# Kernel optimization log

Hardware: AMD Instinct MI355X
Metric: run time of the kernel (lower is better)

The kernel has to match this reference:

```python
import jax, jax.numpy as jnp
import numpy as np

N_NODES = 100000
EPS = 1e-12


def _sage_layer(x, W, b, src, dst):
    # Linear projection: [N, d_in] @ [d_in, d_out]^T
    h = x @ W.T + b
    # F.normalize: row-wise L2 normalize with eps clamp
    norm = jnp.linalg.norm(h, axis=1, keepdims=True)
    h = h / jnp.maximum(norm, EPS)
    # scatter-mean aggregation: message x_j = h[src], reduce at dst
    msg = h[src]                                            # [E, d_out] gather
    agg = jax.ops.segment_sum(msg, dst, num_segments=N_NODES)
    cnt = jax.ops.segment_sum(jnp.ones((dst.shape[0], 1), h.dtype), dst,
                              num_segments=N_NODES)
    return agg / jnp.maximum(cnt, 1.0)
    # NOTE: the torch code does `x += bias` AFTER computing `out` and returns
    # `out`, so the bias parameter of GraphSage never affects the output.


def setup_inputs() -> dict:
    key = jax.random.key(0)
    ks = jax.random.split(key, 12)
    d_in, d_h, d_out = 128, 128, 40
    E = 3200000
    s = lambda k, shape, fan: jax.random.normal(k, shape, jnp.float32) * (1.0 / np.sqrt(fan))
    return {
        "x": jax.random.normal(ks[0], (N_NODES, d_in), jnp.float32),
        "edge_index": jax.random.randint(ks[1], (2, E), 0, N_NODES, jnp.int64),
        "W0": s(ks[2], (d_h, d_in), d_in), "b0": jnp.zeros((d_h,), jnp.float32),
        "W1": s(ks[3], (d_h, d_h), d_h),  "b1": jnp.zeros((d_h,), jnp.float32),
        "W2": s(ks[4], (d_h, d_h), d_h),  "b2": jnp.zeros((d_h,), jnp.float32),
        "Wp1": s(ks[5], (d_h, d_h), d_h), "bp1": jnp.zeros((d_h,), jnp.float32),
        "Wp2": s(ks[6], (d_out, d_h), d_h), "bp2": jnp.zeros((d_out,), jnp.float32),
    }


def reference(x, edge_index, W0, b0, W1, b1, W2, b2, Wp1, bp1, Wp2, bp2):
    src, dst = edge_index[0], edge_index[1]
    h = x
    for W, b in ((W0, b0), (W1, b1), (W2, b2)):
        h = _sage_layer(h, W, b, src, dst)
        h = jax.nn.relu(h)
        # dropout p=0.0 -> identity
    h = h @ Wp1.T + bp1
    h = h @ Wp2.T + bp2
    return jax.nn.log_softmax(h, axis=1)
```

## Files before the change

### kernel.cpp

```cpp
#include <hip/hip_runtime.h>
#include <cmath>

#define NN 100000
#define NB 512
#define NLOC 196
#define CAP 7168
#define CHUNK 8192

typedef unsigned int uint32;
typedef unsigned short ushort16;
typedef __attribute__((ext_vector_type(8))) short short8;
typedef __attribute__((ext_vector_type(4))) float f32x4;
typedef __attribute__((ext_vector_type(2))) float f32x2;

#if defined(__has_builtin)
#if __has_builtin(__builtin_amdgcn_cvt_pk_f32_fp8) && __has_builtin(__builtin_amdgcn_cvt_pk_fp8_f32)
#define HAS_HW_FP8 1
#endif
#endif

__device__ __forceinline__ ushort16 f2bf(float f) {
    uint32 b = __float_as_uint(f);
    uint32 r = (b + 0x7FFFu + ((b >> 16) & 1u)) >> 16;
    return (ushort16)r;
}

#ifdef HAS_HW_FP8
__device__ __forceinline__ uint32 pack4_e4m3(float a, float b, float c, float d) {
    int v = 0;
    v = __builtin_amdgcn_cvt_pk_fp8_f32(a, b, v, false);
    v = __builtin_amdgcn_cvt_pk_fp8_f32(c, d, v, true);
    return (uint32)v;
}
#else
__device__ __forceinline__ uint32 enc1_e4m3(float f) {
    uint32 bits = __float_as_uint(f);
    uint32 s = (bits >> 24) & 0x80u;
    float a = fabsf(f);
    if (a >= 448.f) return s | 0x7Eu;
    if (a < 0.0009765625f) return s;
    if (a < 0.015625f) return s | (uint32)rintf(a * 512.f);
    int e; float m = frexpf(a, &e);
    uint32 q = (uint32)rintf(m * 16.f);
    if (q == 16) { q = 8; e++; }
    return s | ((uint32)(e + 6) << 3) | (q - 8);
}
__device__ __forceinline__ uint32 pack4_e4m3(float a, float b, float c, float d) {
    return enc1_e4m3(a) | (enc1_e4m3(b) << 8) | (enc1_e4m3(c) << 16) | (enc1_e4m3(d) << 24);
}
#endif

#ifdef HAS_HW_FP8
#define DEC_PK(u, w) __builtin_amdgcn_cvt_pk_f32_fp8((int)(u), (w))
#else
__device__ __forceinline__ float dec1_e4m3(uint32 u) {
    uint32 s = (u & 0x80u) << 24;
    uint32 em = u & 0x7Fu;
    if (em >= 8)
        return __uint_as_float(s | (((em >> 3) + 120u) << 23) | ((em & 7u) << 20));
    return ((u & 0x80u) ? -1.f : 1.f) * (float)em * 0.001953125f;
}
__device__ __forceinline__ f32x2 DEC_PK(uint32 u, bool w) {
    uint32 h = w ? (u >> 16) : u;
    f32x2 r; r.x = dec1_e4m3(h & 0xFF); r.y = dec1_e4m3((h >> 8) & 0xFF);
    return r;
}
#endif

__global__ void conv_weights(const float* __restrict__ W0, const float* __restrict__ W1,
                             const float* __restrict__ W2, const float* __restrict__ Wp1,
                             const float* __restrict__ Wp2,
                             uint2* __restrict__ o0, uint2* __restrict__ o1,
                             uint2* __restrict__ o2, uint2* __restrict__ o3,
                             ushort16* __restrict__ o4, int* __restrict__ cursor) {
    int i = blockIdx.x * 256 + threadIdx.x;
    if (i < 16384) {
        const int m = i >> 12;
        const int q = i & 4095;
        const float* src = (m == 0) ? W0 : (m == 1) ? W1 : (m == 2) ? W2 : Wp1;
        uint2* dst = (m == 0) ? o0 : (m == 1) ? o1 : (m == 2) ? o2 : o3;
        const float4 v = *((const float4*)src + q);
        ushort16 o[4] = {f2bf(v.x), f2bf(v.y), f2bf(v.z), f2bf(v.w)};
        dst[q] = *(uint2*)o;
    } else if (i < 16384 + 1536) {
        const int q = i - 16384;
        const int e = q * 4;
        const int j = e >> 7, k = e & 127;
        ushort16 o[4];
#pragma unroll
        for (int c = 0; c < 4; c++) o[c] = (j < 40) ? f2bf(Wp2[j * 128 + k + c]) : (ushort16)0;
        *(uint2*)(o4 + e) = *(uint2*)o;
    } else if (i < 16384 + 1536 + NB) {
        cursor[i - 16384 - 1536] = 0;
    }
}

__global__ __launch_bounds__(512) void csr_k1(const int* __restrict__ srcv,
                                              const int* __restrict__ dstv, int E,
                                              int* __restrict__ cursor,
                                              uint32* __restrict__ ebuf) {
    __shared__ int lhist[NB];
    __shared__ int lstart[NB];
    __shared__ int lbase[NB];
    __shared__ int lcnt[NB];
    __shared__ uint32 sval[CHUNK];
    __shared__ int sgoff[CHUNK];
    const int t = threadIdx.x;
    const int e0 = blockIdx.x * CHUNK;
    const int e1 = min(e0 + CHUNK, E);
    const int n = e1 - e0;

    if (t < NB) { lhist[t] = 0; lcnt[t] = 0; }
    __syncthreads();
    for (int i = e0 + t; i < e1; i += 512)
        atomicAdd(&lhist[dstv[i] / NLOC], 1);
    __syncthreads();

    const int v = lhist[t];
    lstart[t] = v;
    __syncthreads();
    for (int off = 1; off < NB; off <<= 1) {
        int x = (t >= off) ? lstart[t - off] : 0;
        __syncthreads();
        lstart[t] += x;
        __syncthreads();
    }
    const int excl = lstart[t] - v;
    lstart[t] = excl;
    lbase[t] = v ? atomicAdd(&cursor[t], v) : 0;
    __syncthreads();

    for (int i = e0 + t; i < e1; i += 512) {
        const int d = dstv[i];
        const int s = srcv[i];
        const int b = d / NLOC;
        const int pos = atomicAdd(&lcnt[b], 1);
        const int wpos = lbase[b] + pos;
        const int idx = lstart[b] + pos;
        sval[idx] = (uint32)s | ((uint32)(d - b * NLOC) << 17);
        sgoff[idx] = (wpos < CAP) ? (b * CAP + wpos) : -1;
    }
    __syncthreads();

    for (int k = t; k < n; k += 512) {
        const int g = sgoff[k];
        if (g >= 0) ebuf[g] = sval[k];
    }
}

__global__ __launch_bounds__(NB) void scanb_k(const int* __restrict__ cursor,
                                              int* __restrict__ bstart) {
    __shared__ int sd[NB];
    const int t = threadIdx.x;
    const int v = cursor[t];
    sd[t] = v;
    __syncthreads();
    for (int off = 1; off < NB; off <<= 1) {
        int x = (t >= off) ? sd[t - off] : 0;
        __syncthreads();
        sd[t] += x;
        __syncthreads();
    }
    bstart[t] = sd[t] - v;
}

__global__ __launch_bounds__(512) void csr_k2(const uint32* __restrict__ ebuf,
                                              const int* __restrict__ cursor,
                                              const int* __restrict__ bstart,
                                              int* __restrict__ rowptr,
                                              int* __restrict__ colv, int Etot) {
    __shared__ int sd[256];
    __shared__ int loc[256];
    __shared__ int cnt[256];
    __shared__ uint32 eld[CAP];
    __shared__ uint32 sorted[CAP];
    const int b = blockIdx.x;
    const int t = threadIdx.x;
    const int n = min(cursor[b], CAP);
    const int n0 = b * NLOC;
    const int nloc = max(0, min(NN - n0, NLOC));
    const int bst = bstart[b];
    const uint32* seg = ebuf + (size_t)b * CAP;

    if (t < 256) { sd[t] = 0; cnt[t] = 0; }
    __syncthreads();
    for (int i = t; i < n; i += 512) {
        const uint32 p = seg[i];
        eld[i] = p;
        atomicAdd(&sd[p >> 17], 1);
    }
    __syncthreads();
    int v = 0;
    if (t < 256) v = sd[t];
    __syncthreads();
    for (int off = 1; off < 256; off <<= 1) {
        int x = 0;
        if (t < 256 && t >= off) x = sd[t - off];
        __syncthreads();
        if (t < 256) sd[t] += x;
        __syncthreads();
    }
    if (t < 256) loc[t] = sd[t] - v;
    __syncthreads();
    if (t < nloc) rowptr[n0 + t] = bst + loc[t];
    if (b == 0 && t == 0) rowptr[NN] = Etot;

    for (int i = t; i < n; i += 512) {
        const uint32 p = eld[i];
        const int l = p >> 17;
        const int pos = atomicAdd(&cnt[l], 1);
        sorted[loc[l] + pos] = p & 0x1FFFF;
    }
    __syncthreads();
    for (int i = t; i < n; i += 512)
        colv[bst + i] = (int)(sorted[i] << 7);
}

template <int F32IN>
__global__ __launch_bounds__(256) void lin_mfma(const void* __restrict__ Xin,
                                                const ushort16* __restrict__ Wb,
                                                const float* __restrict__ bias,
                                                unsigned char* __restrict__ Y8) {
    __shared__ short8 wls[2048];
    const int t = threadIdx.x;
    const int l = t & 63;
    const int l15 = l & 15, lh = l >> 4;
    const int rbase = blockIdx.x * 64 + (t >> 6) * 16;
    int arow = rbase + l15;
    if (arow >= NN) arow = NN - 1;

#pragma unroll
    for (int it = 0; it < 8; it++) {
        const int idx = it * 256 + t;
        const int j = idx >> 8, kk = (idx >> 6) & 3, ll = idx & 63;
        wls[idx] = *(const short8*)((const ushort16*)Wb + (size_t)(j * 16 + (ll & 15)) * 128 + kk * 32 + (ll >> 4) * 8);
    }

    short8 a[4];
    if (F32IN) {
        const float* ap = (const float*)Xin + (size_t)arow * 128 + lh * 8;
#pragma unroll
        for (int kk = 0; kk < 4; kk++) {
            const float4 p0 = *(const float4*)(ap + kk * 32);
            const float4 p1 = *(const float4*)(ap + kk * 32 + 4);
            ushort16 o[8] = {f2bf(p0.x), f2bf(p0.y), f2bf(p0.z), f2bf(p0.w),
                             f2bf(p1.x), f2bf(p1.y), f2bf(p1.z), f2bf(p1.w)};
            a[kk] = *(short8*)o;
        }
    } else {
        const ushort16* ap = (const ushort16*)Xin + (size_t)arow * 128 + lh * 8;
#pragma unroll
        for (int kk = 0; kk < 4; kk++) a[kk] = *(const short8*)(ap + kk * 32);
    }

    __syncthreads();

    f32x4 acc[8];
#pragma unroll
    for (int j = 0; j < 8; j++) acc[j] = (f32x4){0.f, 0.f, 0.f, 0.f};

#pragma unroll
    for (int kk = 0; kk < 4; kk++)
#pragma unroll
        for (int j = 0; j < 8; j++)
            acc[j] = __builtin_amdgcn_mfma_f32_16x16x32_bf16(wls[j * 256 + kk * 64 + l], a[kk], acc[j], 0, 0, 0);

    float v[8][4];
    float ssq = 0.f;
#pragma unroll
    for (int j = 0; j < 8; j++) {
        const float4 bv = *(const float4*)(bias + j * 16 + lh * 4);
        v[j][0] = acc[j][0] + bv.x;
        v[j][1] = acc[j][1] + bv.y;
        v[j][2] = acc[j][2] + bv.z;
        v[j][3] = acc[j][3] + bv.w;
        ssq += v[j][0] * v[j][0] + v[j][1] * v[j][1] + v[j][2] * v[j][2] + v[j][3] * v[j][3];
    }
    ssq += __shfl_xor(ssq, 16, 64);
    ssq += __shfl_xor(ssq, 32, 64);
    const float sc = 1.f / fmaxf(sqrtf(ssq), 1e-12f);

    const int row = rbase + l15;
    if (row < NN) {
        unsigned char* yp = Y8 + (size_t)row * 128;
#pragma unroll
        for (int j = 0; j < 8; j++) {
            const uint32 p = pack4_e4m3(v[j][0] * sc, v[j][1] * sc, v[j][2] * sc, v[j][3] * sc);
            *(uint32*)(yp + j * 16 + lh * 4) = p;
        }
    }
}

__global__ __launch_bounds__(256) void agg_k(const unsigned char* __restrict__ hp,
                                             const int* __restrict__ rowptr,
                                             const int* __restrict__ colv,
                                             ushort16* __restrict__ outp) {
    const int lane = threadIdx.x & 63;
    const int q = lane >> 4;
    const int l16 = lane & 15;
    const int wid = blockIdx.x * 4 + (threadIdx.x >> 6);
    const int nw = gridDim.x * 4;

    for (int node = wid; node < NN; node += nw) {
        const int s = rowptr[node], e = rowptr[node + 1];
        f32x2 a2[4];
#pragma unroll
        for (int j = 0; j < 4; j++) a2[j] = (f32x2){0.f, 0.f};
        const unsigned char* bp = hp + l16 * 8;

        int i = s + q;
        for (; i + 12 < e; i += 16) {
            const int c0 = colv[i];
            const int c1 = colv[i + 4];
            const int c2 = colv[i + 8];
            const int c3 = colv[i + 12];
            const uint2 u0 = *(const uint2*)(bp + (size_t)(uint32)c0);
            const uint2 u1 = *(const uint2*)(bp + (size_t)(uint32)c1);
            const uint2 u2 = *(const uint2*)(bp + (size_t)(uint32)c2);
            const uint2 u3 = *(const uint2*)(bp + (size_t)(uint32)c3);
#pragma unroll
            for (int r = 0; r < 4; r++) {
                const uint2 u = (r == 0) ? u0 : (r == 1) ? u1 : (r == 2) ? u2 : u3;
                a2[0] += DEC_PK(u.x, false);
                a2[1] += DEC_PK(u.x, true);
                a2[2] += DEC_PK(u.y, false);
                a2[3] += DEC_PK(u.y, true);
            }
        }
        for (; i < e; i += 4) {
            const uint2 u = *(const uint2*)(bp + (size_t)(uint32)colv[i]);
            a2[0] += DEC_PK(u.x, false);
            a2[1] += DEC_PK(u.x, true);
            a2[2] += DEC_PK(u.y, false);
            a2[3] += DEC_PK(u.y, true);
        }

        float av[8] = {a2[0].x, a2[0].y, a2[1].x, a2[1].y,
                       a2[2].x, a2[2].y, a2[3].x, a2[3].y};
#pragma unroll
        for (int j = 0; j < 8; j++) {
            av[j] += __shfl_xor(av[j], 16, 64);
            av[j] += __shfl_xor(av[j], 32, 64);
        }

        if (q == 0) {
            const float inv = 1.f / fmaxf((float)(e - s), 1.f);
            ushort16 o[8];
#pragma unroll
            for (int j = 0; j < 8; j++) o[j] = f2bf(fmaxf(av[j] * inv, 0.f));
            *(uint4*)(outp + (size_t)node * 128 + l16 * 8) = *(uint4*)o;
        }
    }
}

__global__ __launch_bounds__(256) void post_mfma(const ushort16* __restrict__ Bb,
                                                 const ushort16* __restrict__ W1b,
                                                 const float* __restrict__ bp1,
                                                 const ushort16* __restrict__ W2b,
                                                 const float* __restrict__ bp2,
                                                 float* __restrict__ Out) {
    __shared__ ushort16 hls[64 * 128];
    const int t = threadIdx.x;
    const int w = t >> 6;
    const int l = t & 63;
    const int l15 = l & 15, lh = l >> 4;
    const int rl = w * 16 + l15;
    const int rbase = blockIdx.x * 64 + w * 16;
    int arow = rbase + l15;
    if (arow >= NN) arow = NN - 1;

    {
        f32x4 acc[8];
#pragma unroll
        for (int j = 0; j < 8; j++) acc[j] = (f32x4){0.f, 0.f, 0.f, 0.f};
        const ushort16* ap = Bb + (size_t)arow * 128 + lh * 8;
#pragma unroll
        for (int kk = 0; kk < 4; kk++) {
            const short8 a = *(const short8*)(ap + kk * 32);
#pragma unroll
            for (int j = 0; j < 8; j++) {
                const short8 b = *(const short8*)(W1b + (size_t)(j * 16 + l15) * 128 + kk * 32 + lh * 8);
                acc[j] = __builtin_amdgcn_mfma_f32_16x16x32_bf16(b, a, acc[j], 0, 0, 0);
            }
        }
        char* lp = (char*)hls;
#pragma unroll
        for (int j = 0; j < 8; j++) {
            const float4 bv = *(const float4*)(bp1 + j * 16 + lh * 4);
            ushort16 o[4] = {f2bf(acc[j][0] + bv.x), f2bf(acc[j][1] + bv.y),
                             f2bf(acc[j][2] + bv.z), f2bf(acc[j][3] + bv.w)};
            const int byte = (rl * 256 + j * 32 + lh * 8) ^ ((rl & 7) << 4);
            *(uint2*)(lp + byte) = *(uint2*)o;
        }
    }
    __syncthreads();

    {
        f32x4 acc[3];
#pragma unroll
        for (int j = 0; j < 3; j++) acc[j] = (f32x4){0.f, 0.f, 0.f, 0.f};
        const char* lp = (const char*)hls;
#pragma unroll
        for (int kk = 0; kk < 4; kk++) {
            const int byte = (rl * 256 + kk * 64 + lh * 16) ^ ((rl & 7) << 4);
            const short8 a = *(const short8*)(lp + byte);
#pragma unroll
            for (int j = 0; j < 3; j++) {
                const short8 b = *(const short8*)(W2b + (size_t)(j * 16 + l15) * 128 + kk * 32 + lh * 8);
                acc[j] = __builtin_amdgcn_mfma_f32_16x16x32_bf16(b, a, acc[j], 0, 0, 0);
            }
        }

        float v[3][4];
        float m = -1e30f;
#pragma unroll
        for (int j = 0; j < 3; j++) {
            const bool val = (j < 2) || (lh < 2);
            if (val) {
                const float4 bv = *(const float4*)(bp2 + j * 16 + lh * 4);
                v[j][0] = acc[j][0] + bv.x;
                v[j][1] = acc[j][1] + bv.y;
                v[j][2] = acc[j][2] + bv.z;
                v[j][3] = acc[j][3] + bv.w;
#pragma unroll
                for (int r = 0; r < 4; r++) m = fmaxf(m, v[j][r]);
            } else {
#pragma unroll
                for (int r = 0; r < 4; r++) v[j][r] = -1e30f;
            }
        }
        m = fmaxf(m, __shfl_xor(m, 16, 64));
        m = fmaxf(m, __shfl_xor(m, 32, 64));
        float se = 0.f;
#pragma unroll
        for (int j = 0; j < 3; j++)
#pragma unroll
            for (int r = 0; r < 4; r++) se += expf(v[j][r] - m);
        se += __shfl_xor(se, 16, 64);
        se += __shfl_xor(se, 32, 64);
        const float lse = logf(se) + m;

        const int row = rbase + l15;
        if (row < NN) {
            float* op = Out + (size_t)row * 40;
#pragma unroll
            for (int j = 0; j < 3; j++) {
                if (j == 2 && lh >= 2) continue;
                float4 o;
                o.x = v[j][0] - lse; o.y = v[j][1] - lse;
                o.z = v[j][2] - lse; o.w = v[j][3] - lse;
                *(float4*)(op + j * 16 + lh * 4) = o;
            }
        }
    }
}

extern "C" void kernel_launch(void* const* d_in, const int* in_sizes, int n_in,
                              void* d_out, int out_size, void* d_ws, size_t ws_size,
                              hipStream_t stream) {
    const float* x   = (const float*)d_in[0];
    const int*   ei  = (const int*)d_in[1];
    const float* W0  = (const float*)d_in[2];
    const float* b0  = (const float*)d_in[3];
    const float* W1  = (const float*)d_in[4];
    const float* b1  = (const float*)d_in[5];
    const float* W2  = (const float*)d_in[6];
    const float* b2  = (const float*)d_in[7];
    const float* Wp1 = (const float*)d_in[8];
    const float* bp1 = (const float*)d_in[9];
    const float* Wp2 = (const float*)d_in[10];
    const float* bp2 = (const float*)d_in[11];
    float* out = (float*)d_out;

    const int E = in_sizes[1] / 2;
    const int* srcv = ei;
    const int* dstv = ei + E;

    char* w = (char*)d_ws;
    auto alloc = [&](size_t sz) {
        char* p = w;
        w += (sz + 255) & ~(size_t)255;
        return p;
    };
    unsigned char* H8 = (unsigned char*)alloc((size_t)NN * 128);
    ushort16* Bb  = (ushort16*)alloc(sizeof(ushort16) * (size_t)NN * 128);
    uint32* ebuf  = (uint32*)alloc(sizeof(uint32) * (size_t)NB * CAP);
    int*   colv   = (int*)alloc(sizeof(int) * (size_t)E);
    int*   rowptr = (int*)alloc(sizeof(int) * (NN + 1));
    int*   cursor = (int*)alloc(sizeof(int) * NB);
    int*   bstart = (int*)alloc(sizeof(int) * NB);
    ushort16* Wb0 = (ushort16*)alloc(sizeof(ushort16) * 128 * 128);
    ushort16* Wb1 = (ushort16*)alloc(sizeof(ushort16) * 128 * 128);
    ushort16* Wb2 = (ushort16*)alloc(sizeof(ushort16) * 128 * 128);
    ushort16* Wb3 = (ushort16*)alloc(sizeof(ushort16) * 128 * 128);
    ushort16* Wb4 = (ushort16*)alloc(sizeof(ushort16) * 48 * 128);

    conv_weights<<<72, 256, 0, stream>>>(W0, W1, W2, Wp1, Wp2,
                                         (uint2*)Wb0, (uint2*)Wb1, (uint2*)Wb2,
                                         (uint2*)Wb3, Wb4, cursor);

    csr_k1<<<(E + CHUNK - 1) / CHUNK, 512, 0, stream>>>(srcv, dstv, E, cursor, ebuf);
    scanb_k<<<1, NB, 0, stream>>>(cursor, bstart);
    csr_k2<<<NB, 512, 0, stream>>>(ebuf, cursor, bstart, rowptr, colv, E);

    const int nlb = (NN + 63) / 64;
    lin_mfma<1><<<nlb, 256, 0, stream>>>(x, Wb0, b0, H8);
    agg_k<<<4096, 256, 0, stream>>>(H8, rowptr, colv, Bb);
    lin_mfma<0><<<nlb, 256, 0, stream>>>(Bb, Wb1, b1, H8);
    agg_k<<<4096, 256, 0, stream>>>(H8, rowptr, colv, Bb);
    lin_mfma<0><<<nlb, 256, 0, stream>>>(Bb, Wb2, b2, H8);
    agg_k<<<4096, 256, 0, stream>>>(H8, rowptr, colv, Bb);

    post_mfma<<<nlb, 256, 0, stream>>>(Bb, Wb3, bp1, Wb4, bp2, out);
}
```

Baseline: 331.7 us.

## Fuse neighbor aggregation into following linear and post-MLP kernels

Each aggregation step now runs inside the next layer's MFMA kernel. A block gathers and averages its 64 nodes into LDS, then multiplies by the weight tile. This removes the bf16 round trip of the aggregated features through global memory and cuts the kernel count. In exchange, the grid shrinks from 4096 persistent blocks to one block per 64 nodes, with 16 sequential nodes per wave. That may reduce the latency hiding and load balance of the gather.

```diff
diff --git a/kernel.cpp b/kernel.cpp
--- a/kernel.cpp
+++ b/kernel.cpp
@@ -216,11 +216,58 @@
         colv[bst + i] = (int)(sorted[i] << 7);
 }
 
-template <int F32IN>
-__global__ __launch_bounds__(256) void lin_mfma(const void* __restrict__ Xin,
-                                                const ushort16* __restrict__ Wb,
-                                                const float* __restrict__ bias,
-                                                unsigned char* __restrict__ Y8) {
+__device__ __forceinline__ void agg_node(const unsigned char* __restrict__ H8in,
+                                         const int* __restrict__ rowptr,
+                                         const int* __restrict__ colv,
+                                         int node, int l15, int lh,
+                                         float av[8], float& inv) {
+    const int s = rowptr[node], e = rowptr[node + 1];
+    f32x2 a2[4];
+#pragma unroll
+    for (int j = 0; j < 4; j++) a2[j] = (f32x2){0.f, 0.f};
+    const unsigned char* bp = H8in + l15 * 8;
+
+    int i = s + lh;
+    for (; i + 12 < e; i += 16) {
+        const int c0 = colv[i];
+        const int c1 = colv[i + 4];
+        const int c2 = colv[i + 8];
+        const int c3 = colv[i + 12];
+        const uint2 u0 = *(const uint2*)(bp + (size_t)(uint32)c0);
+        const uint2 u1 = *(const uint2*)(bp + (size_t)(uint32)c1);
+        const uint2 u2 = *(const uint2*)(bp + (size_t)(uint32)c2);
+        const uint2 u3 = *(const uint2*)(bp + (size_t)(uint32)c3);
+#pragma unroll
+        for (int r = 0; r < 4; r++) {
+            const uint2 u = (r == 0) ? u0 : (r == 1) ? u1 : (r == 2) ? u2 : u3;
+            a2[0] += DEC_PK(u.x, false);
+            a2[1] += DEC_PK(u.x, true);
+            a2[2] += DEC_PK(u.y, false);
+            a2[3] += DEC_PK(u.y, true);
+        }
+    }
+    for (; i < e; i += 4) {
+        const uint2 u = *(const uint2*)(bp + (size_t)(uint32)colv[i]);
+        a2[0] += DEC_PK(u.x, false);
+        a2[1] += DEC_PK(u.x, true);
+        a2[2] += DEC_PK(u.y, false);
+        a2[3] += DEC_PK(u.y, true);
+    }
+
+    av[0] = a2[0].x; av[1] = a2[0].y; av[2] = a2[1].x; av[3] = a2[1].y;
+    av[4] = a2[2].x; av[5] = a2[2].y; av[6] = a2[3].x; av[7] = a2[3].y;
+#pragma unroll
+    for (int j = 0; j < 8; j++) {
+        av[j] += __shfl_xor(av[j], 16, 64);
+        av[j] += __shfl_xor(av[j], 32, 64);
+    }
+    inv = 1.f / fmaxf((float)(e - s), 1.f);
+}
+
+__global__ __launch_bounds__(256) void lin_mfma0(const float* __restrict__ Xin,
+                                                 const ushort16* __restrict__ Wb,
+                                                 const float* __restrict__ bias,
+                                                 unsigned char* __restrict__ Y8) {
     __shared__ short8 wls[2048];
     const int t = threadIdx.x;
     const int l = t & 63;
@@ -233,12 +280,12 @@
     for (int it = 0; it < 8; it++) {
         const int idx = it * 256 + t;
         const int j = idx >> 8, kk = (idx >> 6) & 3, ll = idx & 63;
-        wls[idx] = *(const short8*)((const ushort16*)Wb + (size_t)(j * 16 + (ll & 15)) * 128 + kk * 32 + (ll >> 4) * 8);
+        wls[idx] = *(const short8*)(Wb + (size_t)(j * 16 + (ll & 15)) * 128 + kk * 32 + (ll >> 4) * 8);
     }
 
     short8 a[4];
-    if (F32IN) {
-        const float* ap = (const float*)Xin + (size_t)arow * 128 + lh * 8;
+    {
+        const float* ap = Xin + (size_t)arow * 128 + lh * 8;
 #pragma unroll
         for (int kk = 0; kk < 4; kk++) {
             const float4 p0 = *(const float4*)(ap + kk * 32);
@@ -247,18 +294,12 @@
                              f2bf(p1.x), f2bf(p1.y), f2bf(p1.z), f2bf(p1.w)};
             a[kk] = *(short8*)o;
         }
-    } else {
-        const ushort16* ap = (const ushort16*)Xin + (size_t)arow * 128 + lh * 8;
-#pragma unroll
-        for (int kk = 0; kk < 4; kk++) a[kk] = *(const short8*)(ap + kk * 32);
-    }
-
+    }
     __syncthreads();
 
     f32x4 acc[8];
 #pragma unroll
     for (int j = 0; j < 8; j++) acc[j] = (f32x4){0.f, 0.f, 0.f, 0.f};
-
 #pragma unroll
     for (int kk = 0; kk < 4; kk++)
 #pragma unroll
@@ -291,74 +332,94 @@
     }
 }
 
-__global__ __launch_bounds__(256) void agg_k(const unsigned char* __restrict__ hp,
-                                             const int* __restrict__ rowptr,
-                                             const int* __restrict__ colv,
-                                             ushort16* __restrict__ outp) {
-    const int lane = threadIdx.x & 63;
-    const int q = lane >> 4;
-    const int l16 = lane & 15;
-    const int wid = blockIdx.x * 4 + (threadIdx.x >> 6);
-    const int nw = gridDim.x * 4;
-
-    for (int node = wid; node < NN; node += nw) {
-        const int s = rowptr[node], e = rowptr[node + 1];
-        f32x2 a2[4];
-#pragma unroll
-        for (int j = 0; j < 4; j++) a2[j] = (f32x2){0.f, 0.f};
-        const unsigned char* bp = hp + l16 * 8;
-
-        int i = s + q;
-        for (; i + 12 < e; i += 16) {
-            const int c0 = colv[i];
-            const int c1 = colv[i + 4];
-            const int c2 = colv[i + 8];
-            const int c3 = colv[i + 12];
-            const uint2 u0 = *(const uint2*)(bp + (size_t)(uint32)c0);
-            const uint2 u1 = *(const uint2*)(bp + (size_t)(uint32)c1);
-            const uint2 u2 = *(const uint2*)(bp + (size_t)(uint32)c2);
-            const uint2 u3 = *(const uint2*)(bp + (size_t)(uint32)c3);
-#pragma unroll
-            for (int r = 0; r < 4; r++) {
-                const uint2 u = (r == 0) ? u0 : (r == 1) ? u1 : (r == 2) ? u2 : u3;
-                a2[0] += DEC_PK(u.x, false);
-                a2[1] += DEC_PK(u.x, true);
-                a2[2] += DEC_PK(u.y, false);
-                a2[3] += DEC_PK(u.y, true);
-            }
-        }
-        for (; i < e; i += 4) {
-            const uint2 u = *(const uint2*)(bp + (size_t)(uint32)colv[i]);
-            a2[0] += DEC_PK(u.x, false);
-            a2[1] += DEC_PK(u.x, true);
-            a2[2] += DEC_PK(u.y, false);
-            a2[3] += DEC_PK(u.y, true);
-        }
-
-        float av[8] = {a2[0].x, a2[0].y, a2[1].x, a2[1].y,
-                       a2[2].x, a2[2].y, a2[3].x, a2[3].y};
+__global__ __launch_bounds__(256) void fused_agg_lin(const unsigned char* __restrict__ H8in,
+                                                     const int* __restrict__ rowptr,
+                                                     const int* __restrict__ colv,
+                                                     const ushort16* __restrict__ Wb,
+                                                     const float* __restrict__ bias,
+                                                     unsigned char* __restrict__ H8out) {
+    __shared__ short8 wls[2048];
+    char* aggls = (char*)wls;
+    const int t = threadIdx.x;
+    const int w = t >> 6;
+    const int l = t & 63;
+    const int l15 = l & 15, lh = l >> 4;
+    const int rbase = blockIdx.x * 64 + w * 16;
+
+    for (int it = 0; it < 16; ++it) {
+        const int node = min(rbase + it, NN - 1);
+        float av[8], inv;
+        agg_node(H8in, rowptr, colv, node, l15, lh, av, inv);
+        if (lh == 0) {
+            ushort16 o[8];
+#pragma unroll
+            for (int j = 0; j < 8; j++) o[j] = f2bf(fmaxf(av[j] * inv, 0.f));
+            const int rl = w * 16 + it;
+            const int byte = (rl * 256 + l15 * 16) ^ ((rl & 7) << 4);
+            *(uint4*)(aggls + byte) = *(uint4*)o;
+        }
+    }
+    __syncthreads();
+
+    const int rl = w * 16 + l15;
+    short8 a[4];
+#pragma unroll
+    for (int kk = 0; kk < 4; kk++)
+        a[kk] = *(const short8*)(aggls + ((rl * 256 + kk * 64 + lh * 16) ^ ((rl & 7) << 4)));
+    __syncthreads();
+
+#pragma unroll
+    for (int it = 0; it < 8; it++) {
+        const int idx = it * 256 + t;
+        const int j = idx >> 8, kk = (idx >> 6) & 3, ll = idx & 63;
+        wls[idx] = *(const short8*)(Wb + (size_t)(j * 16 + (ll & 15)) * 128 + kk * 32 + (ll >> 4) * 8);
+    }
+    __syncthreads();
+
+    f32x4 acc[8];
+#pragma unroll
+    for (int j = 0; j < 8; j++) acc[j] = (f32x4){0.f, 0.f, 0.f, 0.f};
+#pragma unroll
+    for (int kk = 0; kk < 4; kk++)
+#pragma unroll
+        for (int j = 0; j < 8; j++)
+            acc[j] = __builtin_amdgcn_mfma_f32_16x16x32_bf16(wls[j * 256 + kk * 64 + l], a[kk], acc[j], 0, 0, 0);
+
+    float v[8][4];
+    float ssq = 0.f;
+#pragma unroll
+    for (int j = 0; j < 8; j++) {
+        const float4 bv = *(const float4*)(bias + j * 16 + lh * 4);
+        v[j][0] = acc[j][0] + bv.x;
+        v[j][1] = acc[j][1] + bv.y;
+        v[j][2] = acc[j][2] + bv.z;
+        v[j][3] = acc[j][3] + bv.w;
+        ssq += v[j][0] * v[j][0] + v[j][1] * v[j][1] + v[j][2] * v[j][2] + v[j][3] * v[j][3];
+    }
+    ssq += __shfl_xor(ssq, 16, 64);
+    ssq += __shfl_xor(ssq, 32, 64);
+    const float sc = 1.f / fmaxf(sqrtf(ssq), 1e-12f);
+
+    const int row = rbase + l15;
+    if (row < NN) {
+        unsigned char* yp = H8out + (size_t)row * 128;
 #pragma unroll
         for (int j = 0; j < 8; j++) {
-            av[j] += __shfl_xor(av[j], 16, 64);
-            av[j] += __shfl_xor(av[j], 32, 64);
-        }
-
-        if (q == 0) {
-            const float inv = 1.f / fmaxf((float)(e - s), 1.f);
-            ushort16 o[8];
-#pragma unroll
-            for (int j = 0; j < 8; j++) o[j] = f2bf(fmaxf(av[j] * inv, 0.f));
-            *(uint4*)(outp + (size_t)node * 128 + l16 * 8) = *(uint4*)o;
-        }
-    }
-}
-
-__global__ __launch_bounds__(256) void post_mfma(const ushort16* __restrict__ Bb,
-                                                 const ushort16* __restrict__ W1b,
-                                                 const float* __restrict__ bp1,
-                                                 const ushort16* __restrict__ W2b,
-                                                 const float* __restrict__ bp2,
-                                                 float* __restrict__ Out) {
+            const uint32 p = pack4_e4m3(v[j][0] * sc, v[j][1] * sc, v[j][2] * sc, v[j][3] * sc);
+            *(uint32*)(yp + j * 16 + lh * 4) = p;
+        }
+    }
+}
+
+__global__ __launch_bounds__(256) void fused_agg_post(const unsigned char* __restrict__ H8in,
+                                                      const int* __restrict__ rowptr,
+                                                      const int* __restrict__ colv,
+                                                      const ushort16* __restrict__ W1b,
+                                                      const float* __restrict__ bp1,
+                                                      const ushort16* __restrict__ W2b,
+                                                      const float* __restrict__ bp2,
+                                                      float* __restrict__ Out) {
+    __shared__ char aggls[16384];
     __shared__ ushort16 hls[64 * 128];
     const int t = threadIdx.x;
     const int w = t >> 6;
@@ -366,17 +427,29 @@
     const int l15 = l & 15, lh = l >> 4;
     const int rl = w * 16 + l15;
     const int rbase = blockIdx.x * 64 + w * 16;
-    int arow = rbase + l15;
-    if (arow >= NN) arow = NN - 1;
+
+    for (int it = 0; it < 16; ++it) {
+        const int node = min(rbase + it, NN - 1);
+        float av[8], inv;
+        agg_node(H8in, rowptr, colv, node, l15, lh, av, inv);
+        if (lh == 0) {
+            ushort16 o[8];
+#pragma unroll
+            for (int j = 0; j < 8; j++) o[j] = f2bf(fmaxf(av[j] * inv, 0.f));
+            const int r2 = w * 16 + it;
+            const int byte = (r2 * 256 + l15 * 16) ^ ((r2 & 7) << 4);
+            *(uint4*)(aggls + byte) = *(uint4*)o;
+        }
+    }
+    __syncthreads();
 
     {
         f32x4 acc[8];
 #pragma unroll
         for (int j = 0; j < 8; j++) acc[j] = (f32x4){0.f, 0.f, 0.f, 0.f};
-        const ushort16* ap = Bb + (size_t)arow * 128 + lh * 8;
 #pragma unroll
         for (int kk = 0; kk < 4; kk++) {
-            const short8 a = *(const short8*)(ap + kk * 32);
+            const short8 a = *(const short8*)(aggls + ((rl * 256 + kk * 64 + lh * 16) ^ ((rl & 7) << 4)));
 #pragma unroll
             for (int j = 0; j < 8; j++) {
                 const short8 b = *(const short8*)(W1b + (size_t)(j * 16 + l15) * 128 + kk * 32 + lh * 8);
@@ -482,8 +555,8 @@
         w += (sz + 255) & ~(size_t)255;
         return p;
     };
-    unsigned char* H8 = (unsigned char*)alloc((size_t)NN * 128);
-    ushort16* Bb  = (ushort16*)alloc(sizeof(ushort16) * (size_t)NN * 128);
+    unsigned char* H8a = (unsigned char*)alloc((size_t)NN * 128);
+    unsigned char* H8b = (unsigned char*)alloc((size_t)NN * 128);
     uint32* ebuf  = (uint32*)alloc(sizeof(uint32) * (size_t)NB * CAP);
     int*   colv   = (int*)alloc(sizeof(int) * (size_t)E);
     int*   rowptr = (int*)alloc(sizeof(int) * (NN + 1));
@@ -504,12 +577,8 @@
     csr_k2<<<NB, 512, 0, stream>>>(ebuf, cursor, bstart, rowptr, colv, E);
 
     const int nlb = (NN + 63) / 64;
-    lin_mfma<1><<<nlb, 256, 0, stream>>>(x, Wb0, b0, H8);
-    agg_k<<<4096, 256, 0, stream>>>(H8, rowptr, colv, Bb);
-    lin_mfma<0><<<nlb, 256, 0, stream>>>(Bb, Wb1, b1, H8);
-    agg_k<<<4096, 256, 0, stream>>>(H8, rowptr, colv, Bb);
-    lin_mfma<0><<<nlb, 256, 0, stream>>>(Bb, Wb2, b2, H8);
-    agg_k<<<4096, 256, 0, stream>>>(H8, rowptr, colv, Bb);
-
-    post_mfma<<<nlb, 256, 0, stream>>>(Bb, Wb3, bp1, Wb4, bp2, out);
-}
+    lin_mfma0<<<nlb, 256, 0, stream>>>(x, Wb0, b0, H8a);
+    fused_agg_lin<<<nlb, 256, 0, stream>>>(H8a, rowptr, colv, Wb1, b1, H8b);
+    fused_agg_lin<<<nlb, 256, 0, stream>>>(H8b, rowptr, colv, Wb2, b2, H8a);
+    fused_agg_post<<<nlb, 256, 0, stream>>>(H8a, rowptr, colv, Wb3, bp1, Wb4, bp2, out);
+}
```

After: 457.9 us. 38.0% more time.

## Fuse first-layer projection into CSR bucketing kernel to run concurrently

Applied to the files above, without the earlier changes.

Merges the CSR edge-bucketing pass and the first-layer linear+normalize+fp8 projection into one launch, with block ranges split by index, so the independent projection work overlaps the atomic-heavy bucketing. The projection part now uses 512-thread blocks covering 128 rows each. Shared memory becomes dynamic and is sized for the CSR path, which may lower occupancy for the projection blocks. It also saves one kernel launch.

```diff
diff --git a/kernel.cpp b/kernel.cpp
--- a/kernel.cpp
+++ b/kernel.cpp
@@ -95,56 +95,130 @@
     }
 }
 
-__global__ __launch_bounds__(512) void csr_k1(const int* __restrict__ srcv,
-                                              const int* __restrict__ dstv, int E,
-                                              int* __restrict__ cursor,
-                                              uint32* __restrict__ ebuf) {
-    __shared__ int lhist[NB];
-    __shared__ int lstart[NB];
-    __shared__ int lbase[NB];
-    __shared__ int lcnt[NB];
-    __shared__ uint32 sval[CHUNK];
-    __shared__ int sgoff[CHUNK];
+__global__ __launch_bounds__(512) void csr1_lin0(const int* __restrict__ srcv,
+                                                 const int* __restrict__ dstv, int E,
+                                                 int* __restrict__ cursor,
+                                                 uint32* __restrict__ ebuf,
+                                                 const float* __restrict__ Xin,
+                                                 const ushort16* __restrict__ Wb,
+                                                 const float* __restrict__ bias,
+                                                 unsigned char* __restrict__ Y8,
+                                                 int ncsr) {
+    extern __shared__ char smem[];
     const int t = threadIdx.x;
-    const int e0 = blockIdx.x * CHUNK;
-    const int e1 = min(e0 + CHUNK, E);
-    const int n = e1 - e0;
-
-    if (t < NB) { lhist[t] = 0; lcnt[t] = 0; }
-    __syncthreads();
-    for (int i = e0 + t; i < e1; i += 512)
-        atomicAdd(&lhist[dstv[i] / NLOC], 1);
-    __syncthreads();
-
-    const int v = lhist[t];
-    lstart[t] = v;
-    __syncthreads();
-    for (int off = 1; off < NB; off <<= 1) {
-        int x = (t >= off) ? lstart[t - off] : 0;
-        __syncthreads();
-        lstart[t] += x;
-        __syncthreads();
-    }
-    const int excl = lstart[t] - v;
-    lstart[t] = excl;
-    lbase[t] = v ? atomicAdd(&cursor[t], v) : 0;
-    __syncthreads();
-
-    for (int i = e0 + t; i < e1; i += 512) {
-        const int d = dstv[i];
-        const int s = srcv[i];
-        const int b = d / NLOC;
-        const int pos = atomicAdd(&lcnt[b], 1);
-        const int wpos = lbase[b] + pos;
-        const int idx = lstart[b] + pos;
-        sval[idx] = (uint32)s | ((uint32)(d - b * NLOC) << 17);
-        sgoff[idx] = (wpos < CAP) ? (b * CAP + wpos) : -1;
-    }
-    __syncthreads();
-
-    for (int k = t; k < n; k += 512) {
-        const int g = sgoff[k];
-        if (g >= 0) ebuf[g] = sval[k];
+
+    if (blockIdx.x < ncsr) {
+        int* lhist = (int*)smem;
+        int* lstart = lhist + NB;
+        int* lbase = lstart + NB;
+        int* lcnt = lbase + NB;
+        uint32* sval = (uint32*)(lcnt + NB);
+        int* sgoff = (int*)(sval + CHUNK);
+
+        const int e0 = blockIdx.x * CHUNK;
+        const int e1 = min(e0 + CHUNK, E);
+        const int n = e1 - e0;
+
+        if (t < NB) { lhist[t] = 0; lcnt[t] = 0; }
+        __syncthreads();
+        for (int i = e0 + t; i < e1; i += 512)
+            atomicAdd(&lhist[dstv[i] / NLOC], 1);
+        __syncthreads();
+
+        const int v = lhist[t];
+        lstart[t] = v;
+        __syncthreads();
+        for (int off = 1; off < NB; off <<= 1) {
+            int x = (t >= off) ? lstart[t - off] : 0;
+            __syncthreads();
+            lstart[t] += x;
+            __syncthreads();
+        }
+        const int excl = lstart[t] - v;
+        lstart[t] = excl;
+        lbase[t] = v ? atomicAdd(&cursor[t], v) : 0;
+        __syncthreads();
+
+        for (int i = e0 + t; i < e1; i += 512) {
+            const int d = dstv[i];
+            const int s = srcv[i];
+            const int b = d / NLOC;
+            const int pos = atomicAdd(&lcnt[b], 1);
+            const int wpos = lbase[b] + pos;
+            const int idx = lstart[b] + pos;
+            sval[idx] = (uint32)s | ((uint32)(d - b * NLOC) << 17);
+            sgoff[idx] = (wpos < CAP) ? (b * CAP + wpos) : -1;
+        }
+        __syncthreads();
+
+        for (int k = t; k < n; k += 512) {
+            const int g = sgoff[k];
+            if (g >= 0) ebuf[g] = sval[k];
+        }
+    } else {
+        short8* wls = (short8*)smem;
+        const int bid = blockIdx.x - ncsr;
+        const int w = t >> 6;
+        const int l = t & 63;
+        const int l15 = l & 15, lh = l >> 4;
+        const int rbase = bid * 128 + w * 16;
+        int arow = rbase + l15;
+        if (arow >= NN) arow = NN - 1;
+
+#pragma unroll
+        for (int it = 0; it < 4; it++) {
+            const int idx = it * 512 + t;
+            const int j = idx >> 8, kk = (idx >> 6) & 3, ll = idx & 63;
+            wls[idx] = *(const short8*)(Wb + (size_t)(j * 16 + (ll & 15)) * 128 + kk * 32 + (ll >> 4) * 8);
+        }
+
+        short8 a[4];
+        {
+            const float* ap = Xin + (size_t)arow * 128 + lh * 8;
+#pragma unroll
+            for (int kk = 0; kk < 4; kk++) {
+                const float4 p0 = *(const float4*)(ap + kk * 32);
+                const float4 p1 = *(const float4*)(ap + kk * 32 + 4);
+                ushort16 o[8] = {f2bf(p0.x), f2bf(p0.y), f2bf(p0.z), f2bf(p0.w),
+                                 f2bf(p1.x), f2bf(p1.y), f2bf(p1.z), f2bf(p1.w)};
+                a[kk] = *(short8*)o;
+            }
+        }
+        __syncthreads();
+
+        f32x4 acc[8];
+#pragma unroll
+        for (int j = 0; j < 8; j++) acc[j] = (f32x4){0.f, 0.f, 0.f, 0.f};
+#pragma unroll
+        for (int kk = 0; kk < 4; kk++)
+#pragma unroll
+            for (int j = 0; j < 8; j++)
+                acc[j] = __builtin_amdgcn_mfma_f32_16x16x32_bf16(wls[j * 256 + kk * 64 + l], a[kk], acc[j], 0, 0, 0);
+
+        float v[8][4];
+        float ssq = 0.f;
+#pragma unroll
+        for (int j = 0; j < 8; j++) {
+            const float4 bv = *(const float4*)(bias + j * 16 + lh * 4);
+            v[j][0] = acc[j][0] + bv.x;
+            v[j][1] = acc[j][1] + bv.y;
+            v[j][2] = acc[j][2] + bv.z;
+            v[j][3] = acc[j][3] + bv.w;
+            ssq += v[j][0] * v[j][0] + v[j][1] * v[j][1] + v[j][2] * v[j][2] + v[j][3] * v[j][3];
+        }
+        ssq += __shfl_xor(ssq, 16, 64);
+        ssq += __shfl_xor(ssq, 32, 64);
+        const float sc = 1.f / fmaxf(sqrtf(ssq), 1e-12f);
+
+        const int row = rbase + l15;
+        if (row < NN) {
+            unsigned char* yp = Y8 + (size_t)row * 128;
+#pragma unroll
+            for (int j = 0; j < 8; j++) {
+                const uint32 p = pack4_e4m3(v[j][0] * sc, v[j][1] * sc, v[j][2] * sc, v[j][3] * sc);
+                *(uint32*)(yp + j * 16 + lh * 4) = p;
+            }
+        }
     }
 }
 
@@ -216,8 +290,7 @@
         colv[bst + i] = (int)(sorted[i] << 7);
 }
 
-template <int F32IN>
-__global__ __launch_bounds__(256) void lin_mfma(const void* __restrict__ Xin,
+__global__ __launch_bounds__(256) void lin_mfma(const ushort16* __restrict__ Xin,
                                                 const ushort16* __restrict__ Wb,
                                                 const float* __restrict__ bias,
                                                 unsigned char* __restrict__ Y8) {
@@ -233,32 +306,20 @@
     for (int it = 0; it < 8; it++) {
         const int idx = it * 256 + t;
         const int j = idx >> 8, kk = (idx >> 6) & 3, ll = idx & 63;
-        wls[idx] = *(const short8*)((const ushort16*)Wb + (size_t)(j * 16 + (ll & 15)) * 128 + kk * 32 + (ll >> 4) * 8);
+        wls[idx] = *(const short8*)(Wb + (size_t)(j * 16 + (ll & 15)) * 128 + kk * 32 + (ll >> 4) * 8);
     }
 
     short8 a[4];
-    if (F32IN) {
-        const float* ap = (const float*)Xin + (size_t)arow * 128 + lh * 8;
-#pragma unroll
-        for (int kk = 0; kk < 4; kk++) {
-            const float4 p0 = *(const float4*)(ap + kk * 32);
-            const float4 p1 = *(const float4*)(ap + kk * 32 + 4);
-            ushort16 o[8] = {f2bf(p0.x), f2bf(p0.y), f2bf(p0.z), f2bf(p0.w),
-                             f2bf(p1.x), f2bf(p1.y), f2bf(p1.z), f2bf(p1.w)};
-            a[kk] = *(short8*)o;
-        }
-    } else {
-        const ushort16* ap = (const ushort16*)Xin + (size_t)arow * 128 + lh * 8;
+    {
+        const ushort16* ap = Xin + (size_t)arow * 128 + lh * 8;
 #pragma unroll
         for (int kk = 0; kk < 4; kk++) a[kk] = *(const short8*)(ap + kk * 32);
     }
-
     __syncthreads();
 
     f32x4 acc[8];
 #pragma unroll
     for (int j = 0; j < 8; j++) acc[j] = (f32x4){0.f, 0.f, 0.f, 0.f};
-
 #pragma unroll
     for (int kk = 0; kk < 4; kk++)
 #pragma unroll
@@ -499,16 +560,20 @@
                                          (uint2*)Wb0, (uint2*)Wb1, (uint2*)Wb2,
                                          (uint2*)Wb3, Wb4, cursor);
 
-    csr_k1<<<(E + CHUNK - 1) / CHUNK, 512, 0, stream>>>(srcv, dstv, E, cursor, ebuf);
+    const int ncsr = (E + CHUNK - 1) / CHUNK;
+    const int nlin0 = (NN + 127) / 128;
+    const size_t smem = (size_t)(NB * 4 * 4) + (size_t)CHUNK * 8;
+    csr1_lin0<<<ncsr + nlin0, 512, smem, stream>>>(srcv, dstv, E, cursor, ebuf,
+                                                   x, Wb0, b0, H8, ncsr);
+
     scanb_k<<<1, NB, 0, stream>>>(cursor, bstart);
     csr_k2<<<NB, 512, 0, stream>>>(ebuf, cursor, bstart, rowptr, colv, E);
 
     const int nlb = (NN + 63) / 64;
-    lin_mfma<1><<<nlb, 256, 0, stream>>>(x, Wb0, b0, H8);
     agg_k<<<4096, 256, 0, stream>>>(H8, rowptr, colv, Bb);
-    lin_mfma<0><<<nlb, 256, 0, stream>>>(Bb, Wb1, b1, H8);
+    lin_mfma<<<nlb, 256, 0, stream>>>(Bb, Wb1, b1, H8);
     agg_k<<<4096, 256, 0, stream>>>(H8, rowptr, colv, Bb);
-    lin_mfma<0><<<nlb, 256, 0, stream>>>(Bb, Wb2, b2, H8);
+    lin_mfma<<<nlb, 256, 0, stream>>>(Bb, Wb2, b2, H8);
     agg_k<<<4096, 256, 0, stream>>>(H8, rowptr, colv, Bb);
 
     post_mfma<<<nlb, 256, 0, stream>>>(Bb, Wb3, bp1, Wb4, bp2, out);
```

After: 321.9 us. -3.0%, faster.
